# Kernel tuning notes

Hardware: AMD Instinct MI355X
Metric: run time of the kernel (lower is better)

Reference implementation:

```python
import jax, jax.numpy as jnp
import numpy as np

EPS = 1e-5
SLOPE = 0.01  # LeakyReLU default negative_slope


def conv3(x, w):
    # x: [B,C,D,H,W], w: [O,I,3,3,3]; SubMConv3d on a dense grid == dense SAME conv, no bias
    return jax.lax.conv_general_dilated(
        x, w, window_strides=(1, 1, 1), padding='SAME',
        dimension_numbers=('NCDHW', 'OIDHW', 'NCDHW'))


def bn_c(x, g, b, m, v):
    # BatchNorm1d (eval) over channel axis 1 of [B,C,D,H,W]
    s = (1.0, -1, 1, 1, 1)
    return (x - m.reshape(1, -1, 1, 1, 1)) * (g.reshape(1, -1, 1, 1, 1) * jax.lax.rsqrt(v.reshape(1, -1, 1, 1, 1) + EPS)) + b.reshape(1, -1, 1, 1, 1)


def bn_f(x, g, b, m, v):
    # BatchNorm1d (eval) over last (feature) axis
    return (x - m) * (g * jax.lax.rsqrt(v + EPS)) + b


def lrelu(x):
    return jnp.where(x > 0, x, SLOPE * x)


def setup_inputs() -> dict:
    key = jax.random.key(0)
    ks = jax.random.split(key, 32)
    B, C, D, H, W = 2, 256, 64, 64, 16
    N = 100000
    init_size, emb = 32, 3

    fea = jax.random.normal(ks[0], (B, C, D, H, W), dtype=jnp.float32)
    gi0 = jax.random.randint(ks[1], (B, N), 0, D)
    gi1 = jax.random.randint(ks[2], (B, N), 0, H)
    gi2 = jax.random.randint(ks[3], (B, N), 0, W)
    grid_ind = jnp.stack([gi0, gi1, gi2], axis=-1).astype(jnp.int32)  # [B,N,3]
    xyz = jax.random.normal(ks[4], (B, N, 3), dtype=jnp.float32)

    def bn_params(k, c):
        k1, k2, k3, k4 = jax.random.split(k, 4)
        return (1.0 + 0.1 * jax.random.normal(k1, (c,), jnp.float32),
                0.1 * jax.random.normal(k2, (c,), jnp.float32),
                0.1 * jax.random.normal(k3, (c,), jnp.float32),
                0.5 + jax.random.uniform(k4, (c,), jnp.float32))

    W1 = jax.random.normal(ks[5], (C, C, 3, 3, 3), jnp.float32) * (1.0 / np.sqrt(27 * C))
    g1, b1, m1, v1 = bn_params(ks[6], C)
    W2 = jax.random.normal(ks[7], (2 * init_size, C, 3, 3, 3), jnp.float32) * (1.0 / np.sqrt(27 * C))
    g2, b2, m2, v2 = bn_params(ks[8], 2 * init_size)
    W3 = jax.random.normal(ks[9], (init_size, 2 * init_size, 3, 3, 3), jnp.float32) * (1.0 / np.sqrt(27 * 2 * init_size))
    g3, b3, m3, v3 = bn_params(ks[10], init_size)

    Wo1 = jax.random.normal(ks[11], (init_size + 3, init_size), jnp.float32) * (1.0 / np.sqrt(init_size + 3))
    bo1 = 0.01 * jax.random.normal(ks[12], (init_size,), jnp.float32)
    go, bo, mo, vo = bn_params(ks[13], init_size)
    Wo2 = jax.random.normal(ks[14], (init_size, emb), jnp.float32) * (1.0 / np.sqrt(init_size))
    bo2 = 0.01 * jax.random.normal(ks[15], (emb,), jnp.float32)

    return dict(fea=fea, grid_ind=grid_ind, xyz=xyz,
                W1=W1, g1=g1, b1=b1, m1=m1, v1=v1,
                W2=W2, g2=g2, b2=b2, m2=m2, v2=v2,
                W3=W3, g3=g3, b3=b3, m3=m3, v3=v3,
                Wo1=Wo1, bo1=bo1, go=go, bo=bo, mo=mo, vo=vo,
                Wo2=Wo2, bo2=bo2)


def reference(fea, grid_ind, xyz,
              W1, g1, b1, m1, v1,
              W2, g2, b2, m2, v2,
              W3, g3, b3, m3, v3,
              Wo1, bo1, go, bo, mo, vo,
              Wo2, bo2):
    # sparse conv stack (dense-grid equivalent)
    x = lrelu(bn_c(conv3(fea, W1), g1, b1, m1, v1))
    x = lrelu(bn_c(conv3(x, W2), g2, b2, m2, v2))
    x = lrelu(bn_c(conv3(x, W3), g3, b3, m3, v3))  # [B, init_size, D, H, W]

    # fea.dense().permute(0,2,3,4,1) -> [B, D, H, W, C]; per-point gather
    xg = jnp.transpose(x, (0, 2, 3, 4, 1))
    B = xg.shape[0]
    bidx = jnp.arange(B)[:, None]  # [B,1]
    pt = xg[bidx, grid_ind[:, :, 0], grid_ind[:, :, 1], grid_ind[:, :, 2]]  # [B, N, init_size]

    # concat xyz, Linear -> BN -> ReLU -> Linear
    h = jnp.concatenate([pt, xyz[:, :, :3]], axis=-1)
    h = jax.nn.relu(bn_f(h @ Wo1 + bo1, go, bo, mo, vo))
    return h @ Wo2 + bo2  # [B, N, embedding_dim]
```

## Files before the change

### kernel.cpp

```cpp
#include <hip/hip_runtime.h>
#include <stdint.h>

#define EPS 1e-5f
#define SLOPE 0.01f

typedef short bf16x8 __attribute__((ext_vector_type(8)));
typedef float f32x4 __attribute__((ext_vector_type(4)));

__device__ __forceinline__ uint16_t f2bf(float x) {
  union { float f; uint32_t u; } v; v.f = x;
  return (uint16_t)((v.u + 0x7fffu + ((v.u >> 16) & 1u)) >> 16);
}

__device__ __forceinline__ void g2lds16(const void* g, void* l) {
  __builtin_amdgcn_global_load_lds(
      (const __attribute__((address_space(1))) void*)g,
      (__attribute__((address_space(3))) void*)l, 16, 0, 0);
}

__global__ void prep_bn(const float* g1, const float* b1, const float* m1, const float* v1,
                        const float* g2, const float* b2, const float* m2, const float* v2,
                        const float* g3, const float* b3, const float* m3, const float* v3,
                        const float* go, const float* bo, const float* mo, const float* vo,
                        const float* bo1,
                        float* s1, float* be1, float* s2, float* be2,
                        float* s3, float* be3, float* so, float* beo) {
  int t = threadIdx.x;
  if (t < 256) { float s = g1[t] / sqrtf(v1[t] + EPS); s1[t] = s; be1[t] = b1[t] - m1[t] * s; }
  if (t < 64)  { float s = g2[t] / sqrtf(v2[t] + EPS); s2[t] = s; be2[t] = b2[t] - m2[t] * s; }
  if (t < 32)  { float s = g3[t] / sqrtf(v3[t] + EPS); s3[t] = s; be3[t] = b3[t] - m3[t] * s; }
  if (t < 32)  { float s = go[t] / sqrtf(vo[t] + EPS); so[t] = s; beo[t] = bo[t] + (bo1[t] - mo[t]) * s; }
}

__global__ void wtrans(const float* __restrict__ W, uint16_t* __restrict__ Wt,
                       int CO, int CI) {
  int idx = blockIdx.x * 256 + threadIdx.x;
  int total = CO * CI * 27;
  if (idx >= total) return;
  int t = idx / (CO * CI);
  int rem = idx % (CO * CI);
  int co = rem / CI, ci = rem % CI;
  Wt[idx] = f2bf(W[((size_t)co * CI + ci) * 27 + t]);
}

__global__ __launch_bounds__(256) void transpose_fea(const float* __restrict__ fea,
                                                     uint16_t* __restrict__ pad0) {
  __shared__ __align__(16) uint16_t lds[16 * 264];
  int tid = threadIdx.x;
  int idx = blockIdx.x;
  int b = idx >> 12;
  int rem = idx & 4095;
  int d = rem >> 6, h = rem & 63;
  int w = tid & 15, cib = tid >> 4;
  size_t sbase = (size_t)((d * 64 + h) * 16 + w);
#pragma unroll
  for (int p = 0; p < 16; ++p) {
    int ci = p * 16 + cib;
    float v = fea[(size_t)(b * 256 + ci) * 65536 + sbase];
    lds[w * 264 + ci] = f2bf(v);
  }
  __syncthreads();
#pragma unroll
  for (int p = 0; p < 2; ++p) {
    int linear = p * 256 + tid;
    int ww = linear >> 5, c8 = linear & 31;
    uint4 val = *(const uint4*)&lds[ww * 264 + c8 * 8];
    size_t o = ((size_t)b * 78408 + (size_t)((d + 1) * 1188 + (h + 1) * 18 + (ww + 1))) * 256 + c8 * 8;
    *(uint4*)&pad0[o] = val;
  }
}

template <int CI, int CO, int NTILE, int WM, int WN, bool LAST>
__global__ __launch_bounds__(256) void conv_mfma(const uint16_t* __restrict__ padIn,
                                                 const uint16_t* __restrict__ Wt,
                                                 const float* __restrict__ bnS,
                                                 const float* __restrict__ bnB,
                                                 uint16_t* __restrict__ padOut,
                                                 float* __restrict__ x3out) {
  constexpr int MPW = 128 / WM;
  constexpr int NPW = NTILE / WN;
  constexpr int MSUB = MPW / 16;
  constexpr int NSUB = NPW / 16;
  constexpr int BPASS = NTILE / 32;
  constexpr int KC = CI / 64;

  __shared__ __align__(16) uint16_t Alds[128 * 64];
  __shared__ __align__(16) uint16_t Blds[NTILE * 64];

  const int tid = threadIdx.x;
  const int lane = tid & 63;
  const int wv = tid >> 6;
  const int wvm = wv / WN;
  const int wvn = wv % WN;

  const int mt = blockIdx.x;
  const int b = mt >> 9;
  const int r = mt & 511;
  const int d = r >> 3;
  const int h0 = (r & 7) << 3;
  const int n0 = blockIdx.y * NTILE;

  const int subsw = (tid & 7) ^ ((tid >> 3) & 7);
  const int wA = (tid >> 3) & 15;
  const int mhA = tid >> 7;
  const int rowB0 = tid >> 3;

  f32x4 acc[MSUB][NSUB] = {};

  const size_t bOffIn = (size_t)b * 78408 * CI;

  for (int t = 0; t < 27; ++t) {
    const int kd = t / 9, kh = (t / 3) % 3, kw = t % 3;
    const size_t Abase = bOffIn + (size_t)((d + kd) * 1188 + (h0 + kh) * 18 + kw) * CI;
    const size_t Bbase = (size_t)(t * CO + n0) * CI;
    for (int kc = 0; kc < KC; ++kc) {
      __syncthreads();
      {
        const uint16_t* ag = padIn + Abase + kc * 64 + (size_t)wA * CI + subsw * 8;
#pragma unroll
        for (int p = 0; p < 4; ++p)
          g2lds16(ag + (size_t)(mhA + 2 * p) * (18 * CI), (char*)Alds + p * 4096 + wv * 1024);
      }
      {
        const uint16_t* bg = Wt + Bbase + kc * 64 + subsw * 8;
#pragma unroll
        for (int p = 0; p < BPASS; ++p)
          g2lds16(bg + (size_t)(rowB0 + 32 * p) * CI, (char*)Blds + p * 4096 + wv * 1024);
      }
      __syncthreads();
#pragma unroll
      for (int ks = 0; ks < 2; ++ks) {
        bf16x8 af[MSUB], bfr[NSUB];
#pragma unroll
        for (int mi = 0; mi < MSUB; ++mi) {
          int row = wvm * MPW + mi * 16 + (lane & 15);
          int u = (ks * 4 + (lane >> 4)) ^ (row & 7);
          af[mi] = *(const bf16x8*)&Alds[row * 64 + u * 8];
        }
#pragma unroll
        for (int ni = 0; ni < NSUB; ++ni) {
          int row = wvn * NPW + ni * 16 + (lane & 15);
          int u = (ks * 4 + (lane >> 4)) ^ (row & 7);
          bfr[ni] = *(const bf16x8*)&Blds[row * 64 + u * 8];
        }
#pragma unroll
        for (int mi = 0; mi < MSUB; ++mi)
#pragma unroll
          for (int ni = 0; ni < NSUB; ++ni)
            acc[mi][ni] = __builtin_amdgcn_mfma_f32_16x16x32_bf16(af[mi], bfr[ni], acc[mi][ni], 0, 0, 0);
      }
    }
  }

  const int col = lane & 15;
  const int quad = lane >> 4;
#pragma unroll
  for (int ni = 0; ni < NSUB; ++ni) {
    const int co = n0 + wvn * NPW + ni * 16 + col;
    const float sv = bnS[co];
    const float bv = bnB[co];
#pragma unroll
    for (int mi = 0; mi < MSUB; ++mi) {
#pragma unroll
      for (int rr = 0; rr < 4; ++rr) {
        int m = wvm * MPW + mi * 16 + quad * 4 + rr;
        float v = acc[mi][ni][rr] * sv + bv;
        v = v > 0.f ? v : SLOPE * v;
        int mh = m >> 4, w = m & 15;
        if (!LAST) {
          size_t o = ((size_t)b * 78408 +
                      (size_t)((d + 1) * 1188 + (h0 + mh + 1) * 18 + (w + 1))) * CO + co;
          padOut[o] = f2bf(v);
        } else {
          size_t o = ((size_t)b * 65536 + (size_t)((d * 64 + h0 + mh) * 16 + w)) * 32 + co;
          x3out[o] = v;
        }
      }
    }
  }
}

__global__ __launch_bounds__(256) void gather_mlp(const float* __restrict__ x3,
                                                  const int* __restrict__ gidx,
                                                  const float* __restrict__ xyz,
                                                  const float* __restrict__ Wo1,
                                                  const float* __restrict__ so,
                                                  const float* __restrict__ beo,
                                                  const float* __restrict__ Wo2,
                                                  const float* __restrict__ bo2,
                                                  float* __restrict__ out) {
  __shared__ __align__(16) float w1[35 * 32];
  __shared__ float w2[32 * 3];
  __shared__ float sS[32], sB[32], b2s[3];
  int tid = threadIdx.x;
  for (int i = tid; i < 1120; i += 256) w1[i] = Wo1[i];
  if (tid < 96) w2[tid] = Wo2[tid];
  if (tid < 32) { sS[tid] = so[tid]; sB[tid] = beo[tid]; }
  if (tid < 3) b2s[tid] = bo2[tid];
  __syncthreads();

  int idx = blockIdx.x * 256 + tid;
  if (idx >= 200000) return;
  int b = idx >= 100000 ? 1 : 0;
  int gb = idx * 3;
  int i0 = gidx[gb], i1 = gidx[gb + 1], i2 = gidx[gb + 2];
  const float* pt = x3 + ((size_t)b * 65536 + (size_t)((i0 * 64 + i1) * 16 + i2)) * 32;

  float h[35];
#pragma unroll
  for (int q = 0; q < 8; ++q) {
    float4 v = *(const float4*)(pt + q * 4);
    h[q * 4] = v.x; h[q * 4 + 1] = v.y; h[q * 4 + 2] = v.z; h[q * 4 + 3] = v.w;
  }
  h[32] = xyz[gb]; h[33] = xyz[gb + 1]; h[34] = xyz[gb + 2];

  float a[32];
#pragma unroll
  for (int j = 0; j < 32; ++j) a[j] = 0.f;
#pragma unroll
  for (int k = 0; k < 35; ++k) {
    float hk = h[k];
    const float4* wr = (const float4*)(w1 + k * 32);
#pragma unroll
    for (int q = 0; q < 8; ++q) {
      float4 wv = wr[q];
      a[q * 4 + 0] += hk * wv.x;
      a[q * 4 + 1] += hk * wv.y;
      a[q * 4 + 2] += hk * wv.z;
      a[q * 4 + 3] += hk * wv.w;
    }
  }
  float o0 = b2s[0], o1 = b2s[1], o2 = b2s[2];
#pragma unroll
  for (int j = 0; j < 32; ++j) {
    float y = a[j] * sS[j] + sB[j];
    y = y > 0.f ? y : 0.f;
    o0 += y * w2[j * 3 + 0];
    o1 += y * w2[j * 3 + 1];
    o2 += y * w2[j * 3 + 2];
  }
  out[gb] = o0; out[gb + 1] = o1; out[gb + 2] = o2;
}

extern "C" void kernel_launch(void* const* d_in, const int* in_sizes, int n_in,
                              void* d_out, int out_size, void* d_ws, size_t ws_size,
                              hipStream_t stream) {
  (void)in_sizes; (void)n_in; (void)out_size;
  if (ws_size < 165130000) return;

  const float* fea = (const float*)d_in[0];
  const int*   gidx = (const int*)d_in[1];
  const float* xyz = (const float*)d_in[2];
  const float* W1 = (const float*)d_in[3];
  const float* g1 = (const float*)d_in[4];
  const float* b1 = (const float*)d_in[5];
  const float* m1 = (const float*)d_in[6];
  const float* v1 = (const float*)d_in[7];
  const float* W2 = (const float*)d_in[8];
  const float* g2 = (const float*)d_in[9];
  const float* b2 = (const float*)d_in[10];
  const float* m2 = (const float*)d_in[11];
  const float* v2 = (const float*)d_in[12];
  const float* W3 = (const float*)d_in[13];
  const float* g3 = (const float*)d_in[14];
  const float* b3 = (const float*)d_in[15];
  const float* m3 = (const float*)d_in[16];
  const float* v3 = (const float*)d_in[17];
  const float* Wo1 = (const float*)d_in[18];
  const float* bo1 = (const float*)d_in[19];
  const float* go = (const float*)d_in[20];
  const float* bo = (const float*)d_in[21];
  const float* mo = (const float*)d_in[22];
  const float* vo = (const float*)d_in[23];
  const float* Wo2 = (const float*)d_in[24];
  const float* bo2 = (const float*)d_in[25];

  char* ws = (char*)d_ws;
  uint16_t* pad0 = (uint16_t*)(ws);
  uint16_t* pad1 = (uint16_t*)(ws + 80289792);
  uint16_t* Wt1 = (uint16_t*)(ws + 160579584);
  uint16_t* Wt2 = (uint16_t*)(ws + 164118528);
  uint16_t* Wt3 = (uint16_t*)(ws + 165003264);
  float* s1  = (float*)(ws + 165113856 + 0 * 1024);
  float* be1 = (float*)(ws + 165113856 + 1 * 1024);
  float* s2  = (float*)(ws + 165113856 + 2 * 1024);
  float* be2 = (float*)(ws + 165113856 + 3 * 1024);
  float* s3  = (float*)(ws + 165113856 + 4 * 1024);
  float* be3 = (float*)(ws + 165113856 + 5 * 1024);
  float* so  = (float*)(ws + 165113856 + 6 * 1024);
  float* beo = (float*)(ws + 165113856 + 7 * 1024);
  uint16_t* pad2 = (uint16_t*)(ws);
  float* x3 = (float*)(ws + 20072448);

  hipMemsetAsync(ws, 0, 160579584, stream);

  prep_bn<<<1, 256, 0, stream>>>(g1, b1, m1, v1, g2, b2, m2, v2, g3, b3, m3, v3,
                                 go, bo, mo, vo, bo1, s1, be1, s2, be2, s3, be3, so, beo);
  wtrans<<<6912, 256, 0, stream>>>(W1, Wt1, 256, 256);
  wtrans<<<1728, 256, 0, stream>>>(W2, Wt2, 64, 256);
  wtrans<<<216, 256, 0, stream>>>(W3, Wt3, 32, 64);
  transpose_fea<<<8192, 256, 0, stream>>>(fea, pad0);

  conv_mfma<256, 256, 128, 2, 2, false>
      <<<dim3(1024, 2), 256, 0, stream>>>(pad0, Wt1, s1, be1, pad1, nullptr);

  hipMemsetAsync(pad2, 0, 20072448, stream);

  conv_mfma<256, 64, 64, 2, 2, false>
      <<<dim3(1024, 1), 256, 0, stream>>>(pad1, Wt2, s2, be2, pad2, nullptr);

  conv_mfma<64, 32, 32, 4, 1, true>
      <<<dim3(1024, 1), 256, 0, stream>>>(pad2, Wt3, s3, be3, nullptr, x3);

  gather_mlp<<<782, 256, 0, stream>>>(x3, gidx, xyz, Wo1, so, beo, Wo2, bo2, (float*)d_out);
}
```

Measured before the change: 1.095 ms.

## Reuse A halo tile across kw taps in conv and simplify fea transpose

The conv kernel now loads an 8x18-wide padded input row slab (with halo) once per (kd,kh,kc) and reuses it for all three kw offsets, instead of reloading a 128-row A tile for each of the 27 taps. This cuts global-to-LDS traffic for A by about a factor of three, at the cost of a different LDS layout and swizzle, plus barrier overhead on each kw step. Separately, transpose_fea drops its LDS staging: each thread reads 128 channels strided by the spatial size and writes 16-byte packed bf16 chunks directly, with fewer blocks launched.

```diff
diff --git a/kernel.cpp b/kernel.cpp
--- a/kernel.cpp
+++ b/kernel.cpp
@@ -45,28 +45,24 @@
 
 __global__ __launch_bounds__(256) void transpose_fea(const float* __restrict__ fea,
                                                      uint16_t* __restrict__ pad0) {
-  __shared__ __align__(16) uint16_t lds[16 * 264];
   int tid = threadIdx.x;
   int idx = blockIdx.x;
-  int b = idx >> 12;
-  int rem = idx & 4095;
-  int d = rem >> 6, h = rem & 63;
-  int w = tid & 15, cib = tid >> 4;
-  size_t sbase = (size_t)((d * 64 + h) * 16 + w);
-#pragma unroll
-  for (int p = 0; p < 16; ++p) {
-    int ci = p * 16 + cib;
-    float v = fea[(size_t)(b * 256 + ci) * 65536 + sbase];
-    lds[w * 264 + ci] = f2bf(v);
-  }
-  __syncthreads();
-#pragma unroll
-  for (int p = 0; p < 2; ++p) {
-    int linear = p * 256 + tid;
-    int ww = linear >> 5, c8 = linear & 31;
-    uint4 val = *(const uint4*)&lds[ww * 264 + c8 * 8];
-    size_t o = ((size_t)b * 78408 + (size_t)((d + 1) * 1188 + (h + 1) * 18 + (ww + 1))) * 256 + c8 * 8;
-    *(uint4*)&pad0[o] = val;
+  int half = idx & 1;
+  int q = (idx >> 1) & 3;
+  int d = (idx >> 3) & 63;
+  int b = idx >> 9;
+  int s = q * 256 + tid;
+  int h = s >> 4, w = s & 15;
+  const float* src = fea + (size_t)(b * 256 + half * 128) * 65536 + (size_t)d * 1024 + s;
+  uint16_t* dst = pad0 + ((size_t)b * 78408 +
+                          (size_t)((d + 1) * 1188 + (h + 1) * 18 + (w + 1))) * 256 + half * 128;
+#pragma unroll 4
+  for (int c8 = 0; c8 < 16; ++c8) {
+    uint16_t v[8];
+#pragma unroll
+    for (int j = 0; j < 8; ++j)
+      v[j] = f2bf(src[(size_t)(c8 * 8 + j) * 65536]);
+    *(uint4*)&dst[c8 * 8] = *(uint4*)v;
   }
 }
 
@@ -84,7 +80,7 @@
   constexpr int BPASS = NTILE / 32;
   constexpr int KC = CI / 64;
 
-  __shared__ __align__(16) uint16_t Alds[128 * 64];
+  __shared__ __align__(16) uint16_t Alds[20 * 8 * 64];
   __shared__ __align__(16) uint16_t Blds[NTILE * 64];
 
   const int tid = threadIdx.x;
@@ -100,54 +96,58 @@
   const int h0 = (r & 7) << 3;
   const int n0 = blockIdx.y * NTILE;
 
-  const int subsw = (tid & 7) ^ ((tid >> 3) & 7);
-  const int wA = (tid >> 3) & 15;
-  const int mhA = tid >> 7;
+  const int subswB = (tid & 7) ^ ((tid >> 3) & 7);
   const int rowB0 = tid >> 3;
+  const int mhA = lane >> 3;
+  const int unA = lane & 7;
 
   f32x4 acc[MSUB][NSUB] = {};
 
   const size_t bOffIn = (size_t)b * 78408 * CI;
 
-  for (int t = 0; t < 27; ++t) {
-    const int kd = t / 9, kh = (t / 3) % 3, kw = t % 3;
-    const size_t Abase = bOffIn + (size_t)((d + kd) * 1188 + (h0 + kh) * 18 + kw) * CI;
-    const size_t Bbase = (size_t)(t * CO + n0) * CI;
+  for (int dh = 0; dh < 9; ++dh) {
+    const int kd = dh / 3, kh = dh % 3;
+    const size_t Abase = bOffIn + (size_t)((d + kd) * 1188 + (h0 + kh) * 18) * CI;
     for (int kc = 0; kc < KC; ++kc) {
-      __syncthreads();
-      {
-        const uint16_t* ag = padIn + Abase + kc * 64 + (size_t)wA * CI + subsw * 8;
-#pragma unroll
-        for (int p = 0; p < 4; ++p)
-          g2lds16(ag + (size_t)(mhA + 2 * p) * (18 * CI), (char*)Alds + p * 4096 + wv * 1024);
-      }
-      {
-        const uint16_t* bg = Wt + Bbase + kc * 64 + subsw * 8;
-#pragma unroll
-        for (int p = 0; p < BPASS; ++p)
-          g2lds16(bg + (size_t)(rowB0 + 32 * p) * CI, (char*)Blds + p * 4096 + wv * 1024);
-      }
-      __syncthreads();
-#pragma unroll
-      for (int ks = 0; ks < 2; ++ks) {
-        bf16x8 af[MSUB], bfr[NSUB];
-#pragma unroll
-        for (int mi = 0; mi < MSUB; ++mi) {
-          int row = wvm * MPW + mi * 16 + (lane & 15);
-          int u = (ks * 4 + (lane >> 4)) ^ (row & 7);
-          af[mi] = *(const bf16x8*)&Alds[row * 64 + u * 8];
+      for (int kw = 0; kw < 3; ++kw) {
+        __syncthreads();
+        if (kw == 0) {
+          const uint16_t* ag = padIn + Abase + kc * 64 + (size_t)mhA * (18 * CI);
+#pragma unroll
+          for (int p = 0; p < 5; ++p) {
+            int wp = wv * 5 + p;
+            int gu = unA ^ (wp & 7);
+            g2lds16(ag + (size_t)wp * CI + gu * 8, (char*)Alds + wp * 1024);
+          }
         }
-#pragma unroll
-        for (int ni = 0; ni < NSUB; ++ni) {
-          int row = wvn * NPW + ni * 16 + (lane & 15);
-          int u = (ks * 4 + (lane >> 4)) ^ (row & 7);
-          bfr[ni] = *(const bf16x8*)&Blds[row * 64 + u * 8];
+        {
+          const uint16_t* bg = Wt + (size_t)((dh * 3 + kw) * CO + n0) * CI + kc * 64 + subswB * 8;
+#pragma unroll
+          for (int p = 0; p < BPASS; ++p)
+            g2lds16(bg + (size_t)(rowB0 + 32 * p) * CI, (char*)Blds + p * 4096 + wv * 1024);
         }
-#pragma unroll
-        for (int mi = 0; mi < MSUB; ++mi)
-#pragma unroll
-          for (int ni = 0; ni < NSUB; ++ni)
-            acc[mi][ni] = __builtin_amdgcn_mfma_f32_16x16x32_bf16(af[mi], bfr[ni], acc[mi][ni], 0, 0, 0);
+        __syncthreads();
+#pragma unroll
+        for (int ks = 0; ks < 2; ++ks) {
+          bf16x8 af[MSUB], bfr[NSUB];
+#pragma unroll
+          for (int mi = 0; mi < MSUB; ++mi) {
+            int wq = (lane & 15) + kw;
+            int u = (ks * 4 + (lane >> 4)) ^ (wq & 7);
+            af[mi] = *(const bf16x8*)&Alds[wq * 512 + (wvm * MSUB + mi) * 64 + u * 8];
+          }
+#pragma unroll
+          for (int ni = 0; ni < NSUB; ++ni) {
+            int row = wvn * NPW + ni * 16 + (lane & 15);
+            int u = (ks * 4 + (lane >> 4)) ^ (row & 7);
+            bfr[ni] = *(const bf16x8*)&Blds[row * 64 + u * 8];
+          }
+#pragma unroll
+          for (int mi = 0; mi < MSUB; ++mi)
+#pragma unroll
+            for (int ni = 0; ni < NSUB; ++ni)
+              acc[mi][ni] = __builtin_amdgcn_mfma_f32_16x16x32_bf16(af[mi], bfr[ni], acc[mi][ni], 0, 0, 0);
+        }
       }
     }
   }
@@ -299,7 +299,7 @@
   wtrans<<<6912, 256, 0, stream>>>(W1, Wt1, 256, 256);
   wtrans<<<1728, 256, 0, stream>>>(W2, Wt2, 64, 256);
   wtrans<<<216, 256, 0, stream>>>(W3, Wt3, 32, 64);
-  transpose_fea<<<8192, 256, 0, stream>>>(fea, pad0);
+  transpose_fea<<<1024, 256, 0, stream>>>(fea, pad0);
 
   conv_mfma<256, 256, 128, 2, 2, false>
       <<<dim3(1024, 2), 256, 0, stream>>>(pad0, Wt1, s1, be1, pad1, nullptr);
```

Measured after the change: 1.046 ms. 4.5% less time.
